# Kernel tuning notes

Hardware: AMD Instinct MI355X
Metric: run time of the kernel (lower is better)

Reference implementation:

```python
import jax, jax.numpy as jnp
import numpy as np

N6 = 524288          # nodes at depth 6 (full-octree batch of 2)
N5 = N6 // 8         # 65536 nodes at depth 5
N4 = N5 // 8         # 8192 nodes at depth 4
EPS = 1e-5           # torch BatchNorm1d default eps


def _pool(x):
    # octree_max_pool on a full octree: 8 contiguous children -> parent max
    n, c = x.shape
    return jnp.max(x.reshape(n // 8, 8, c), axis=1)


def _up(x):
    # octree_upsample on a full octree: each parent broadcast to its 8 children
    return jnp.repeat(x, 8, axis=0)


def _conv1x1_bn_relu(x, w, g, b):
    # Conv1x1 (Linear, no bias) + BatchNorm1d (training-mode batch stats) + ReLU
    y = x @ w                              # [N, Cout]
    m = jnp.mean(y, axis=0)
    v = jnp.var(y, axis=0)                 # biased variance, as in torch BN
    y = (y - m) * jax.lax.rsqrt(v + EPS) * g + b
    return jax.nn.relu(y)


def setup_inputs() -> dict:
    key = jax.random.key(0)
    ks = jax.random.split(key, 8)
    s = 0.02
    return {
        "data0": jax.random.normal(ks[0], (N6, 96), jnp.float32),
        "data1": jax.random.normal(ks[1], (N5, 192), jnp.float32),
        "w01": jax.random.normal(ks[2], (96, 192), jnp.float32) * s,
        "g01": jnp.ones((192,), jnp.float32),
        "b01": jnp.zeros((192,), jnp.float32),
        "w02": jax.random.normal(ks[3], (96, 384), jnp.float32) * s,
        "g02": jnp.ones((384,), jnp.float32),
        "b02": jnp.zeros((384,), jnp.float32),
        "w10": jax.random.normal(ks[4], (192, 96), jnp.float32) * s,
        "g10": jnp.ones((96,), jnp.float32),
        "b10": jnp.zeros((96,), jnp.float32),
        "w12": jax.random.normal(ks[5], (192, 384), jnp.float32) * s,
        "g12": jnp.ones((384,), jnp.float32),
        "b12": jnp.zeros((384,), jnp.float32),
        "depth": 6,
    }


def reference(data0, data1, w01, g01, b01, w02, g02, b02,
              w10, g10, b10, w12, g12, b12, depth):
    # channels = [96, 192, 384]; data0 at depth, data1 at depth-1.
    # out[j] = sum_i TransFunc(channels[i]->channels[j])(data[i], depth-i -> depth-j)
    # j=0 (depth, 96ch):   identity(data0) + upsample(conv10(data1))
    out0 = data0 + _up(_conv1x1_bn_relu(data1, w10, g10, b10))
    # j=1 (depth-1, 192ch): conv01(pool(data0)) + identity(data1)
    p0 = _pool(data0)                      # [N5, 96]
    out1 = _conv1x1_bn_relu(p0, w01, g01, b01) + data1
    # j=2 (depth-2, 384ch): conv02(pool^2(data0)) + conv12(pool(data1))
    out2 = (_conv1x1_bn_relu(_pool(p0), w02, g02, b02)
            + _conv1x1_bn_relu(_pool(data1), w12, g12, b12))
    return (out0, out1, out2)
```

## Files before the change

kernel.cpp:

```cpp
#include <hip/hip_runtime.h>

typedef unsigned short u16;
typedef __attribute__((ext_vector_type(8))) short short8;
typedef __attribute__((ext_vector_type(4))) float f4;
typedef __attribute__((ext_vector_type(4))) unsigned short u16x4;

#define CN6 524288
#define CN5 65536
#define CN4 8192

__device__ inline u16 f2bf(float f){
  unsigned u = __float_as_uint(f);
  return (u16)((u + 0x7FFFu + ((u >> 16) & 1u)) >> 16);
}
__device__ inline float bf2f(u16 h){ return __uint_as_float(((unsigned)h) << 16); }

__device__ inline f4 nt_load4(const float* p){
  return __builtin_nontemporal_load(reinterpret_cast<const f4*>(p));
}
__device__ inline void nt_store4(float* p, f4 v){
  __builtin_nontemporal_store(v, reinterpret_cast<f4*>(p));
}


__global__ __launch_bounds__(256) void k_prep(const float* __restrict__ w10, const float* __restrict__ w01,
                                              const float* __restrict__ w02, const float* __restrict__ w12,
                                              u16* __restrict__ wT10, u16* __restrict__ wT01,
                                              u16* __restrict__ wT02, u16* __restrict__ wT12,
                                              float* __restrict__ stats){
  int i = blockIdx.x * 256 + threadIdx.x;
  if (i < 2112) stats[i] = 0.f;
  if (i < 18432){ int j = i / 192, k = i - j * 192; wT10[i] = f2bf(w10[k * 96 + j]); }
  else if (i < 36864){ int e = i - 18432; int j = e / 96, k = e - j * 96; wT01[e] = f2bf(w01[k * 192 + j]); }
  else if (i < 73728){ int e = i - 36864; int j = e / 96, k = e - j * 96; wT02[e] = f2bf(w02[k * 384 + j]); }
  else if (i < 147456){ int e = i - 73728; int j = e / 192, k = e - j * 192; wT12[e] = f2bf(w12[k * 384 + j]); }
}

__global__ __launch_bounds__(256) void k_gemm10p(const float* __restrict__ d1, const u16* __restrict__ wT10,
                                                 u16* __restrict__ y10, u16* __restrict__ p1){
  __shared__ u16 sm[64 * 200];
  int tid = threadIdx.x, bid = blockIdx.x;

  if (tid < 192){
    int p = tid / 24, c8 = tid - p * 24;
    f4 v0[8], v1[8];
    #pragma unroll
    for (int r = 0; r < 8; r++){
      const float* src = d1 + ((size_t)bid * 64 + p * 8 + r) * 192 + c8 * 8;
      v0[r] = *reinterpret_cast<const f4*>(src);
      v1[r] = *reinterpret_cast<const f4*>(src + 4);
    }
    float mx[8];
    #pragma unroll
    for (int q = 0; q < 4; q++){ mx[q] = v0[0][q]; mx[4 + q] = v1[0][q]; }
    #pragma unroll
    for (int r = 0; r < 8; r++){
      short8 h;
      #pragma unroll
      for (int q = 0; q < 4; q++){
        h[q]     = (short)f2bf(v0[r][q]);
        h[4 + q] = (short)f2bf(v1[r][q]);
        if (r){ mx[q] = fmaxf(mx[q], v0[r][q]); mx[4 + q] = fmaxf(mx[4 + q], v1[r][q]); }
      }
      *reinterpret_cast<short8*>(&sm[(p * 8 + r) * 200 + c8 * 8]) = h;
    }
    short8 hp;
    #pragma unroll
    for (int q = 0; q < 8; q++) hp[q] = (short)f2bf(mx[q]);
    *reinterpret_cast<short8*>(p1 + ((size_t)bid * 8 + p) * 192 + c8 * 8) = hp;
  }
  __syncthreads();

  int lane = tid & 63, wave = tid >> 6;
  int colb = lane & 15;
  int k0 = (lane >> 4) * 8, rgrp = (lane >> 4) * 4;
  int arowl = wave * 16 + colb;
  short8 xf[6];
  #pragma unroll
  for (int s = 0; s < 6; s++) xf[s] = *reinterpret_cast<short8*>(&sm[arowl * 200 + s * 32 + k0]);

  size_t xrow = (size_t)bid * 64 + arowl;
  #pragma unroll
  for (int j = 0; j < 6; j++){
    f4 acc = {0.f, 0.f, 0.f, 0.f};
    const u16* wr = wT10 + (size_t)(j * 16 + colb) * 192 + k0;
    #pragma unroll
    for (int s = 0; s < 6; s++)
      acc = __builtin_amdgcn_mfma_f32_16x16x32_bf16(*reinterpret_cast<const short8*>(wr + s * 32), xf[s], acc, 0, 0, 0);
    u16x4 h;
    #pragma unroll
    for (int r = 0; r < 4; r++) h[r] = f2bf(acc[r]);
    *reinterpret_cast<u16x4*>(y10 + xrow * 96 + j * 16 + rgrp) = h;
  }
}

__global__ __launch_bounds__(192) void k_stats10(const u16* __restrict__ y10, float* __restrict__ stats){
  __shared__ float ls[96], lq[96];
  int tid = threadIdx.x, bid = blockIdx.x;
  if (tid < 96){ ls[tid] = 0.f; lq[tid] = 0.f; }
  __syncthreads();
  int c8 = tid % 12, rl = tid / 12;
  float s1[8], s2[8];
  #pragma unroll
  for (int q = 0; q < 8; q++){ s1[q] = 0.f; s2[q] = 0.f; }
  for (int it = 0; it < 32; it++){
    size_t row = (size_t)bid * 512 + it * 16 + rl;
    short8 h = *reinterpret_cast<const short8*>(y10 + row * 96 + c8 * 8);
    #pragma unroll
    for (int q = 0; q < 8; q++){
      float v = bf2f((u16)h[q]);
      s1[q] += v; s2[q] += v * v;
    }
  }
  #pragma unroll
  for (int q = 0; q < 8; q++){
    atomicAdd(&ls[c8 * 8 + q], s1[q]);
    atomicAdd(&lq[c8 * 8 + q], s2[q]);
  }
  __syncthreads();
  if (tid < 96){ atomicAdd(&stats[tid], ls[tid]); atomicAdd(&stats[1056 + tid], lq[tid]); }
}

__global__ __launch_bounds__(256) void k_out0(const float* __restrict__ d0, const u16* __restrict__ y10,
                                              const float* __restrict__ stats,
                                              const float* __restrict__ g10, const float* __restrict__ b10,
                                              float* __restrict__ out0, u16* __restrict__ p0, u16* __restrict__ p00){
  __shared__ float yv[8][96];
  __shared__ float sd[64][100];
  __shared__ float sp[8][96];
  int tid = threadIdx.x, gp = blockIdx.x;

  if (tid < 192){
    int p = tid / 24, c4 = tid - p * 24;
    u16x4 yb = *reinterpret_cast<const u16x4*>(y10 + ((size_t)gp * 8 + p) * 96 + c4 * 4);
    f4 o;
    #pragma unroll
    for (int q = 0; q < 4; q++){
      int c = c4 * 4 + q;
      float m = stats[c] * (1.f / 65536.f);
      float vv = stats[1056 + c] * (1.f / 65536.f) - m * m;
      float a = g10[c] * rsqrtf(vv + 1e-5f);
      float cc = b10[c] - m * a;
      o[q] = fmaxf(bf2f((u16)yb[q]) * a + cc, 0.f);
    }
    *reinterpret_cast<f4*>(&yv[p][c4 * 4]) = o;
  }
  __syncthreads();

  const float* dsrc = d0 + (size_t)gp * 6144;
  float* ddst = out0 + (size_t)gp * 6144;
  f4 v[6];
  #pragma unroll
  for (int i = 0; i < 6; i++) v[i] = nt_load4(dsrc + (i * 256 + tid) * 4);
  #pragma unroll
  for (int i = 0; i < 6; i++){
    int idx = i * 256 + tid;
    int row = idx / 24, c4 = idx - row * 24;
    f4 y = *reinterpret_cast<f4*>(&yv[row >> 3][c4 * 4]);
    f4 o;
    #pragma unroll
    for (int q = 0; q < 4; q++) o[q] = v[i][q] + y[q];
    nt_store4(ddst + idx * 4, o);
    *reinterpret_cast<f4*>(&sd[row][c4 * 4]) = v[i];
  }
  __syncthreads();

  if (tid < 192){
    int p = tid / 24, c4 = tid - p * 24;
    f4 m = *reinterpret_cast<f4*>(&sd[p * 8][c4 * 4]);
    #pragma unroll
    for (int r = 1; r < 8; r++){
      f4 x = *reinterpret_cast<f4*>(&sd[p * 8 + r][c4 * 4]);
      #pragma unroll
      for (int q = 0; q < 4; q++) m[q] = fmaxf(m[q], x[q]);
    }
    u16x4 h;
    #pragma unroll
    for (int q = 0; q < 4; q++) h[q] = f2bf(m[q]);
    *reinterpret_cast<u16x4*>(p0 + ((size_t)gp * 8 + p) * 96 + c4 * 4) = h;
    *reinterpret_cast<f4*>(&sp[p][c4 * 4]) = m;
  }
  __syncthreads();
  if (tid < 24){
    f4 m = *reinterpret_cast<f4*>(&sp[0][tid * 4]);
    #pragma unroll
    for (int pp = 1; pp < 8; pp++){
      f4 x = *reinterpret_cast<f4*>(&sp[pp][tid * 4]);
      #pragma unroll
      for (int q = 0; q < 4; q++) m[q] = fmaxf(m[q], x[q]);
    }
    u16x4 h;
    #pragma unroll
    for (int q = 0; q < 4; q++) h[q] = f2bf(m[q]);
    *reinterpret_cast<u16x4*>(p00 + (size_t)gp * 96 + tid * 4) = h;
  }
}

template<int Ci, int Co>
__device__ __forceinline__ void stats_body(const u16* __restrict__ x, const u16* __restrict__ wT,
                                           float* __restrict__ sum, float* __restrict__ sq,
                                           int bid, float* ls, float* lq){
  int tid = threadIdx.x;
  for (int t = tid; t < Co; t += 256){ ls[t] = 0.f; lq[t] = 0.f; }
  __syncthreads();
  int lane = tid & 63, wave = tid >> 6;
  int arow = bid * 64 + wave * 16 + (lane & 15);
  int k0 = (lane >> 4) * 8;
  constexpr int KS = Ci / 32;
  short8 af[KS];
  const u16* xr = x + (size_t)arow * Ci + k0;
  #pragma unroll
  for (int s = 0; s < KS; s++) af[s] = *reinterpret_cast<const short8*>(xr + s * 32);
  int colb = lane & 15;
  #pragma unroll 4
  for (int j = 0; j < Co / 16; j++){
    int col = j * 16 + colb;
    f4 acc = {0.f, 0.f, 0.f, 0.f};
    const u16* wr = wT + (size_t)col * Ci + k0;
    #pragma unroll
    for (int s = 0; s < KS; s++)
      acc = __builtin_amdgcn_mfma_f32_16x16x32_bf16(af[s], *reinterpret_cast<const short8*>(wr + s * 32), acc, 0, 0, 0);
    float s1 = acc[0] + acc[1] + acc[2] + acc[3];
    float s2 = acc[0]*acc[0] + acc[1]*acc[1] + acc[2]*acc[2] + acc[3]*acc[3];
    atomicAdd(&ls[col], s1);
    atomicAdd(&lq[col], s2);
  }
  __syncthreads();
  for (int t = tid; t < Co; t += 256){ atomicAdd(&sum[t], ls[t]); atomicAdd(&sq[t], lq[t]); }
}

__global__ __launch_bounds__(256) void k_statsAll(const u16* __restrict__ p0, const u16* __restrict__ p00,
                                                  const u16* __restrict__ p1,
                                                  const u16* __restrict__ wT01, const u16* __restrict__ wT02,
                                                  const u16* __restrict__ wT12, float* __restrict__ stats){
  __shared__ float ls[384], lq[384];
  int bid = blockIdx.x;
  if (bid < 1024)      stats_body<96, 192>(p0,  wT01, stats + 96,  stats + 1056 + 96,  bid,        ls, lq);
  else if (bid < 1152) stats_body<96, 384>(p00, wT02, stats + 288, stats + 1056 + 288, bid - 1024, ls, lq);
  else                 stats_body<192,384>(p1,  wT12, stats + 672, stats + 1056 + 672, bid - 1152, ls, lq);
}

__global__ __launch_bounds__(256) void k_out1(const u16* __restrict__ p0, const u16* __restrict__ wT01,
                                              const float* __restrict__ d1, const float* __restrict__ stats,
                                              const float* __restrict__ g01, const float* __restrict__ b01,
                                              float* __restrict__ out1){
  __shared__ float aL[192], cL[192];
  __shared__ float so[64 * 196];
  int tid = threadIdx.x, bid = blockIdx.x;
  if (tid < 192){
    float m = stats[96 + tid] * (1.f / 65536.f);
    float v = stats[1056 + 96 + tid] * (1.f / 65536.f) - m * m;
    float a = g01[tid] * rsqrtf(v + 1e-5f);
    aL[tid] = a; cL[tid] = b01[tid] - m * a;
  }
  __syncthreads();
  int lane = tid & 63, wave = tid >> 6;
  int colb = lane & 15;
  int k0 = (lane >> 4) * 8, rgrp = (lane >> 4) * 4;
  int rowl = wave * 16 + colb;
  short8 xf[3];
  const u16* xr = p0 + ((size_t)bid * 64 + rowl) * 96 + k0;
  #pragma unroll
  for (int s = 0; s < 3; s++) xf[s] = *reinterpret_cast<const short8*>(xr + s * 32);
  #pragma unroll 4
  for (int j = 0; j < 12; j++){
    int ch0 = j * 16 + rgrp;
    f4 acc = {0.f, 0.f, 0.f, 0.f};
    const u16* wr = wT01 + (size_t)(j * 16 + colb) * 96 + k0;
    #pragma unroll
    for (int s = 0; s < 3; s++)
      acc = __builtin_amdgcn_mfma_f32_16x16x32_bf16(*reinterpret_cast<const short8*>(wr + s * 32), xf[s], acc, 0, 0, 0);
    f4 o;
    #pragma unroll
    for (int r = 0; r < 4; r++){
      int ch = ch0 + r;
      o[r] = fmaxf(acc[r] * aL[ch] + cL[ch], 0.f);
    }
    *reinterpret_cast<f4*>(&so[rowl * 196 + ch0]) = o;
  }
  __syncthreads();
  const float* d1b = d1 + (size_t)bid * 64 * 192;
  float* o1b = out1 + (size_t)bid * 64 * 192;
  #pragma unroll
  for (int i = 0; i < 12; i++){
    int idx = i * 256 + tid;
    int rl = idx / 48, c4i = idx % 48;
    f4 y = *reinterpret_cast<f4*>(&so[rl * 196 + c4i * 4]);
    int off = rl * 192 + c4i * 4;
    f4 g = nt_load4(d1b + off);
    f4 o;
    #pragma unroll
    for (int q = 0; q < 4; q++) o[q] = y[q] + g[q];
    nt_store4(o1b + off, o);
  }
}

__global__ __launch_bounds__(256) void k_out2(const u16* __restrict__ p00, const u16* __restrict__ p1,
                                              const u16* __restrict__ wT02, const u16* __restrict__ wT12,
                                              const float* __restrict__ stats,
                                              const float* __restrict__ g02, const float* __restrict__ b02,
                                              const float* __restrict__ g12, const float* __restrict__ b12,
                                              float* __restrict__ out2){
  __shared__ float a2[384], c2[384], a1[384], c1[384];
  __shared__ float so[32 * 392];
  int tid = threadIdx.x, bid = blockIdx.x;
  for (int t = tid; t < 384; t += 256){
    float m = stats[288 + t] * (1.f / 8192.f);
    float v = stats[1056 + 288 + t] * (1.f / 8192.f) - m * m;
    float a = g02[t] * rsqrtf(v + 1e-5f);
    a2[t] = a; c2[t] = b02[t] - m * a;
    m = stats[672 + t] * (1.f / 8192.f);
    v = stats[1056 + 672 + t] * (1.f / 8192.f) - m * m;
    a = g12[t] * rsqrtf(v + 1e-5f);
    a1[t] = a; c1[t] = b12[t] - m * a;
  }
  __syncthreads();
  int lane = tid & 63, wave = tid >> 6;
  int wr2 = wave >> 1, wc = wave & 1;
  int colb = lane & 15;
  int k0 = (lane >> 4) * 8, rgrp = (lane >> 4) * 4;
  int rowl = wr2 * 16 + colb;
  size_t arow = (size_t)bid * 32 + rowl;
  short8 xA[3], xB[6];
  #pragma unroll
  for (int s = 0; s < 3; s++) xA[s] = *reinterpret_cast<const short8*>(p00 + arow * 96 + k0 + s * 32);
  #pragma unroll
  for (int s = 0; s < 6; s++) xB[s] = *reinterpret_cast<const short8*>(p1 + arow * 192 + k0 + s * 32);
  #pragma unroll 2
  for (int j = 0; j < 12; j++){
    int ch0 = wc * 192 + j * 16 + rgrp;
    int wrow = wc * 192 + j * 16 + colb;
    f4 u = {0.f, 0.f, 0.f, 0.f}, w = {0.f, 0.f, 0.f, 0.f};
    const u16* wra = wT02 + (size_t)wrow * 96 + k0;
    #pragma unroll
    for (int s = 0; s < 3; s++)
      u = __builtin_amdgcn_mfma_f32_16x16x32_bf16(*reinterpret_cast<const short8*>(wra + s * 32), xA[s], u, 0, 0, 0);
    const u16* wrb = wT12 + (size_t)wrow * 192 + k0;
    #pragma unroll
    for (int s = 0; s < 6; s++)
      w = __builtin_amdgcn_mfma_f32_16x16x32_bf16(*reinterpret_cast<const short8*>(wrb + s * 32), xB[s], w, 0, 0, 0);
    f4 o;
    #pragma unroll
    for (int r = 0; r < 4; r++){
      int ch = ch0 + r;
      o[r] = fmaxf(u[r] * a2[ch] + c2[ch], 0.f) + fmaxf(w[r] * a1[ch] + c1[ch], 0.f);
    }
    *reinterpret_cast<f4*>(&so[rowl * 392 + ch0]) = o;
  }
  __syncthreads();
  #pragma unroll
  for (int i = 0; i < 12; i++){
    int idx = i * 256 + tid;
    int rl = idx / 96, c4i = idx % 96;
    f4 v = *reinterpret_cast<f4*>(&so[rl * 392 + c4i * 4]);
    nt_store4(out2 + ((size_t)bid * 32 + rl) * 384 + c4i * 4, v);
  }
}

extern "C" void kernel_launch(void* const* d_in, const int* in_sizes, int n_in,
                              void* d_out, int out_size, void* d_ws, size_t ws_size,
                              hipStream_t stream){
  const float* data0 = (const float*)d_in[0];
  const float* data1 = (const float*)d_in[1];
  const float* w01 = (const float*)d_in[2];
  const float* g01 = (const float*)d_in[3];
  const float* b01 = (const float*)d_in[4];
  const float* w02 = (const float*)d_in[5];
  const float* g02 = (const float*)d_in[6];
  const float* b02 = (const float*)d_in[7];
  const float* w10 = (const float*)d_in[8];
  const float* g10 = (const float*)d_in[9];
  const float* b10 = (const float*)d_in[10];
  const float* w12 = (const float*)d_in[11];
  const float* g12 = (const float*)d_in[12];
  const float* b12 = (const float*)d_in[13];

  float* out0 = (float*)d_out;
  float* out1 = out0 + (size_t)CN6 * 96;
  float* out2 = out1 + (size_t)CN5 * 192;

  char* ws = (char*)d_ws;
  u16* p1   = (u16*)(ws + 0);
  u16* p0   = (u16*)(ws + 3145728);
  u16* p00  = (u16*)(ws + 15728640);
  u16* y10  = (u16*)(ws + 17301504);
  u16* wT10 = (u16*)(ws + 29884416);
  u16* wT01 = (u16*)(ws + 29921280);
  u16* wT02 = (u16*)(ws + 29958144);
  u16* wT12 = (u16*)(ws + 30031872);
  float* stats = (float*)(ws + 30179328);

  k_prep<<<576, 256, 0, stream>>>(w10, w01, w02, w12, wT10, wT01, wT02, wT12, stats);
  k_gemm10p<<<1024, 256, 0, stream>>>(data1, wT10, y10, p1);
  k_stats10<<<128, 192, 0, stream>>>(y10, stats);
  k_out0<<<8192, 256, 0, stream>>>(data0, y10, stats, g10, b10, out0, p0, p00);
  k_statsAll<<<1280, 256, 0, stream>>>(p0, p00, p1, wT01, wT02, wT12, stats);
  k_out1<<<1024, 256, 0, stream>>>(p0, wT01, data1, stats, g01, b01, out1);
  k_out2<<<256, 256, 0, stream>>>(p00, p1, wT02, wT12, stats, g02, b02, g12, b12, out2);
}
```

Baseline: 213.8 us.

## Merge out1/out2 kernels, widen stats10 grid, reduce LDS atomics via shuffles

Combines the out1 and out2 kernels into one launch, with the block index selecting the branch and a shared-memory union, so one launch is saved and the two small grids can run concurrently. The k_stats10 grid grows from 128 to 1024 blocks, each covering 64 rows, to improve occupancy at the cost of more global atomics. In stats_body, per-column partial sums are combined with cross-lane shuffles before the shared-memory atomics, cutting LDS atomic traffic fourfold. The merged kernel's LDS footprint is the larger of the two branches, which may lower occupancy for the out1 blocks.

```diff
diff --git a/kernel.cpp b/kernel.cpp
--- a/kernel.cpp
+++ b/kernel.cpp
@@ -103,8 +103,9 @@
   float s1[8], s2[8];
   #pragma unroll
   for (int q = 0; q < 8; q++){ s1[q] = 0.f; s2[q] = 0.f; }
-  for (int it = 0; it < 32; it++){
-    size_t row = (size_t)bid * 512 + it * 16 + rl;
+  #pragma unroll
+  for (int it = 0; it < 4; it++){
+    size_t row = (size_t)bid * 64 + it * 16 + rl;
     short8 h = *reinterpret_cast<const short8*>(y10 + row * 96 + c8 * 8);
     #pragma unroll
     for (int q = 0; q < 8; q++){
@@ -222,8 +223,12 @@
       acc = __builtin_amdgcn_mfma_f32_16x16x32_bf16(af[s], *reinterpret_cast<const short8*>(wr + s * 32), acc, 0, 0, 0);
     float s1 = acc[0] + acc[1] + acc[2] + acc[3];
     float s2 = acc[0]*acc[0] + acc[1]*acc[1] + acc[2]*acc[2] + acc[3]*acc[3];
-    atomicAdd(&ls[col], s1);
-    atomicAdd(&lq[col], s2);
+    s1 += __shfl_xor(s1, 16); s1 += __shfl_xor(s1, 32);
+    s2 += __shfl_xor(s2, 16); s2 += __shfl_xor(s2, 32);
+    if ((lane >> 4) == 0){
+      atomicAdd(&ls[col], s1);
+      atomicAdd(&lq[col], s2);
+    }
   }
   __syncthreads();
   for (int t = tid; t < Co; t += 256){ atomicAdd(&sum[t], ls[t]); atomicAdd(&sq[t], lq[t]); }
@@ -240,120 +245,123 @@
   else                 stats_body<192,384>(p1,  wT12, stats + 672, stats + 1056 + 672, bid - 1152, ls, lq);
 }
 
-__global__ __launch_bounds__(256) void k_out1(const u16* __restrict__ p0, const u16* __restrict__ wT01,
-                                              const float* __restrict__ d1, const float* __restrict__ stats,
-                                              const float* __restrict__ g01, const float* __restrict__ b01,
-                                              float* __restrict__ out1){
-  __shared__ float aL[192], cL[192];
-  __shared__ float so[64 * 196];
-  int tid = threadIdx.x, bid = blockIdx.x;
-  if (tid < 192){
-    float m = stats[96 + tid] * (1.f / 65536.f);
-    float v = stats[1056 + 96 + tid] * (1.f / 65536.f) - m * m;
-    float a = g01[tid] * rsqrtf(v + 1e-5f);
-    aL[tid] = a; cL[tid] = b01[tid] - m * a;
-  }
-  __syncthreads();
-  int lane = tid & 63, wave = tid >> 6;
-  int colb = lane & 15;
-  int k0 = (lane >> 4) * 8, rgrp = (lane >> 4) * 4;
-  int rowl = wave * 16 + colb;
-  short8 xf[3];
-  const u16* xr = p0 + ((size_t)bid * 64 + rowl) * 96 + k0;
-  #pragma unroll
-  for (int s = 0; s < 3; s++) xf[s] = *reinterpret_cast<const short8*>(xr + s * 32);
-  #pragma unroll 4
-  for (int j = 0; j < 12; j++){
-    int ch0 = j * 16 + rgrp;
-    f4 acc = {0.f, 0.f, 0.f, 0.f};
-    const u16* wr = wT01 + (size_t)(j * 16 + colb) * 96 + k0;
-    #pragma unroll
-    for (int s = 0; s < 3; s++)
-      acc = __builtin_amdgcn_mfma_f32_16x16x32_bf16(*reinterpret_cast<const short8*>(wr + s * 32), xf[s], acc, 0, 0, 0);
-    f4 o;
-    #pragma unroll
-    for (int r = 0; r < 4; r++){
-      int ch = ch0 + r;
-      o[r] = fmaxf(acc[r] * aL[ch] + cL[ch], 0.f);
-    }
-    *reinterpret_cast<f4*>(&so[rowl * 196 + ch0]) = o;
-  }
-  __syncthreads();
-  const float* d1b = d1 + (size_t)bid * 64 * 192;
-  float* o1b = out1 + (size_t)bid * 64 * 192;
-  #pragma unroll
-  for (int i = 0; i < 12; i++){
-    int idx = i * 256 + tid;
-    int rl = idx / 48, c4i = idx % 48;
-    f4 y = *reinterpret_cast<f4*>(&so[rl * 196 + c4i * 4]);
-    int off = rl * 192 + c4i * 4;
-    f4 g = nt_load4(d1b + off);
-    f4 o;
-    #pragma unroll
-    for (int q = 0; q < 4; q++) o[q] = y[q] + g[q];
-    nt_store4(o1b + off, o);
-  }
-}
-
-__global__ __launch_bounds__(256) void k_out2(const u16* __restrict__ p00, const u16* __restrict__ p1,
-                                              const u16* __restrict__ wT02, const u16* __restrict__ wT12,
-                                              const float* __restrict__ stats,
-                                              const float* __restrict__ g02, const float* __restrict__ b02,
-                                              const float* __restrict__ g12, const float* __restrict__ b12,
-                                              float* __restrict__ out2){
-  __shared__ float a2[384], c2[384], a1[384], c1[384];
-  __shared__ float so[32 * 392];
-  int tid = threadIdx.x, bid = blockIdx.x;
-  for (int t = tid; t < 384; t += 256){
-    float m = stats[288 + t] * (1.f / 8192.f);
-    float v = stats[1056 + 288 + t] * (1.f / 8192.f) - m * m;
-    float a = g02[t] * rsqrtf(v + 1e-5f);
-    a2[t] = a; c2[t] = b02[t] - m * a;
-    m = stats[672 + t] * (1.f / 8192.f);
-    v = stats[1056 + 672 + t] * (1.f / 8192.f) - m * m;
-    a = g12[t] * rsqrtf(v + 1e-5f);
-    a1[t] = a; c1[t] = b12[t] - m * a;
-  }
-  __syncthreads();
-  int lane = tid & 63, wave = tid >> 6;
-  int wr2 = wave >> 1, wc = wave & 1;
-  int colb = lane & 15;
-  int k0 = (lane >> 4) * 8, rgrp = (lane >> 4) * 4;
-  int rowl = wr2 * 16 + colb;
-  size_t arow = (size_t)bid * 32 + rowl;
-  short8 xA[3], xB[6];
-  #pragma unroll
-  for (int s = 0; s < 3; s++) xA[s] = *reinterpret_cast<const short8*>(p00 + arow * 96 + k0 + s * 32);
-  #pragma unroll
-  for (int s = 0; s < 6; s++) xB[s] = *reinterpret_cast<const short8*>(p1 + arow * 192 + k0 + s * 32);
-  #pragma unroll 2
-  for (int j = 0; j < 12; j++){
-    int ch0 = wc * 192 + j * 16 + rgrp;
-    int wrow = wc * 192 + j * 16 + colb;
-    f4 u = {0.f, 0.f, 0.f, 0.f}, w = {0.f, 0.f, 0.f, 0.f};
-    const u16* wra = wT02 + (size_t)wrow * 96 + k0;
-    #pragma unroll
-    for (int s = 0; s < 3; s++)
-      u = __builtin_amdgcn_mfma_f32_16x16x32_bf16(*reinterpret_cast<const short8*>(wra + s * 32), xA[s], u, 0, 0, 0);
-    const u16* wrb = wT12 + (size_t)wrow * 192 + k0;
-    #pragma unroll
-    for (int s = 0; s < 6; s++)
-      w = __builtin_amdgcn_mfma_f32_16x16x32_bf16(*reinterpret_cast<const short8*>(wrb + s * 32), xB[s], w, 0, 0, 0);
-    f4 o;
-    #pragma unroll
-    for (int r = 0; r < 4; r++){
-      int ch = ch0 + r;
-      o[r] = fmaxf(u[r] * a2[ch] + c2[ch], 0.f) + fmaxf(w[r] * a1[ch] + c1[ch], 0.f);
-    }
-    *reinterpret_cast<f4*>(&so[rowl * 392 + ch0]) = o;
-  }
-  __syncthreads();
-  #pragma unroll
-  for (int i = 0; i < 12; i++){
-    int idx = i * 256 + tid;
-    int rl = idx / 96, c4i = idx % 96;
-    f4 v = *reinterpret_cast<f4*>(&so[rl * 392 + c4i * 4]);
-    nt_store4(out2 + ((size_t)bid * 32 + rl) * 384 + c4i * 4, v);
+union ShOut {
+  struct { float aL[192], cL[192], so[64 * 196]; } o1;
+  struct { float a2[384], c2[384], a1[384], c1[384], so2[32 * 392]; } o2;
+};
+
+__global__ __launch_bounds__(256) void k_outfinal(const u16* __restrict__ p0, const u16* __restrict__ wT01,
+                                                  const float* __restrict__ d1,
+                                                  const u16* __restrict__ p00, const u16* __restrict__ p1,
+                                                  const u16* __restrict__ wT02, const u16* __restrict__ wT12,
+                                                  const float* __restrict__ stats,
+                                                  const float* __restrict__ g01, const float* __restrict__ b01,
+                                                  const float* __restrict__ g02, const float* __restrict__ b02,
+                                                  const float* __restrict__ g12, const float* __restrict__ b12,
+                                                  float* __restrict__ out1, float* __restrict__ out2){
+  __shared__ ShOut sh;
+  int tid = threadIdx.x;
+  if (blockIdx.x < 1024){
+    int bid = blockIdx.x;
+    if (tid < 192){
+      float m = stats[96 + tid] * (1.f / 65536.f);
+      float v = stats[1056 + 96 + tid] * (1.f / 65536.f) - m * m;
+      float a = g01[tid] * rsqrtf(v + 1e-5f);
+      sh.o1.aL[tid] = a; sh.o1.cL[tid] = b01[tid] - m * a;
+    }
+    __syncthreads();
+    int lane = tid & 63, wave = tid >> 6;
+    int colb = lane & 15;
+    int k0 = (lane >> 4) * 8, rgrp = (lane >> 4) * 4;
+    int rowl = wave * 16 + colb;
+    short8 xf[3];
+    const u16* xr = p0 + ((size_t)bid * 64 + rowl) * 96 + k0;
+    #pragma unroll
+    for (int s = 0; s < 3; s++) xf[s] = *reinterpret_cast<const short8*>(xr + s * 32);
+    #pragma unroll 4
+    for (int j = 0; j < 12; j++){
+      int ch0 = j * 16 + rgrp;
+      f4 acc = {0.f, 0.f, 0.f, 0.f};
+      const u16* wr = wT01 + (size_t)(j * 16 + colb) * 96 + k0;
+      #pragma unroll
+      for (int s = 0; s < 3; s++)
+        acc = __builtin_amdgcn_mfma_f32_16x16x32_bf16(*reinterpret_cast<const short8*>(wr + s * 32), xf[s], acc, 0, 0, 0);
+      f4 o;
+      #pragma unroll
+      for (int r = 0; r < 4; r++){
+        int ch = ch0 + r;
+        o[r] = fmaxf(acc[r] * sh.o1.aL[ch] + sh.o1.cL[ch], 0.f);
+      }
+      *reinterpret_cast<f4*>(&sh.o1.so[rowl * 196 + ch0]) = o;
+    }
+    __syncthreads();
+    const float* d1b = d1 + (size_t)bid * 64 * 192;
+    float* o1b = out1 + (size_t)bid * 64 * 192;
+    #pragma unroll
+    for (int i = 0; i < 12; i++){
+      int idx = i * 256 + tid;
+      int rl = idx / 48, c4i = idx % 48;
+      f4 y = *reinterpret_cast<f4*>(&sh.o1.so[rl * 196 + c4i * 4]);
+      int off = rl * 192 + c4i * 4;
+      f4 g = nt_load4(d1b + off);
+      f4 o;
+      #pragma unroll
+      for (int q = 0; q < 4; q++) o[q] = y[q] + g[q];
+      nt_store4(o1b + off, o);
+    }
+  } else {
+    int bid = blockIdx.x - 1024;
+    for (int t = tid; t < 384; t += 256){
+      float m = stats[288 + t] * (1.f / 8192.f);
+      float v = stats[1056 + 288 + t] * (1.f / 8192.f) - m * m;
+      float a = g02[t] * rsqrtf(v + 1e-5f);
+      sh.o2.a2[t] = a; sh.o2.c2[t] = b02[t] - m * a;
+      m = stats[672 + t] * (1.f / 8192.f);
+      v = stats[1056 + 672 + t] * (1.f / 8192.f) - m * m;
+      a = g12[t] * rsqrtf(v + 1e-5f);
+      sh.o2.a1[t] = a; sh.o2.c1[t] = b12[t] - m * a;
+    }
+    __syncthreads();
+    int lane = tid & 63, wave = tid >> 6;
+    int wr2 = wave >> 1, wc = wave & 1;
+    int colb = lane & 15;
+    int k0 = (lane >> 4) * 8, rgrp = (lane >> 4) * 4;
+    int rowl = wr2 * 16 + colb;
+    size_t arow = (size_t)bid * 32 + rowl;
+    short8 xA[3], xB[6];
+    #pragma unroll
+    for (int s = 0; s < 3; s++) xA[s] = *reinterpret_cast<const short8*>(p00 + arow * 96 + k0 + s * 32);
+    #pragma unroll
+    for (int s = 0; s < 6; s++) xB[s] = *reinterpret_cast<const short8*>(p1 + arow * 192 + k0 + s * 32);
+    #pragma unroll 2
+    for (int j = 0; j < 12; j++){
+      int ch0 = wc * 192 + j * 16 + rgrp;
+      int wrow = wc * 192 + j * 16 + colb;
+      f4 u = {0.f, 0.f, 0.f, 0.f}, w = {0.f, 0.f, 0.f, 0.f};
+      const u16* wra = wT02 + (size_t)wrow * 96 + k0;
+      #pragma unroll
+      for (int s = 0; s < 3; s++)
+        u = __builtin_amdgcn_mfma_f32_16x16x32_bf16(*reinterpret_cast<const short8*>(wra + s * 32), xA[s], u, 0, 0, 0);
+      const u16* wrb = wT12 + (size_t)wrow * 192 + k0;
+      #pragma unroll
+      for (int s = 0; s < 6; s++)
+        w = __builtin_amdgcn_mfma_f32_16x16x32_bf16(*reinterpret_cast<const short8*>(wrb + s * 32), xB[s], w, 0, 0, 0);
+      f4 o;
+      #pragma unroll
+      for (int r = 0; r < 4; r++){
+        int ch = ch0 + r;
+        o[r] = fmaxf(u[r] * sh.o2.a2[ch] + sh.o2.c2[ch], 0.f) + fmaxf(w[r] * sh.o2.a1[ch] + sh.o2.c1[ch], 0.f);
+      }
+      *reinterpret_cast<f4*>(&sh.o2.so2[rowl * 392 + ch0]) = o;
+    }
+    __syncthreads();
+    #pragma unroll
+    for (int i = 0; i < 12; i++){
+      int idx = i * 256 + tid;
+      int rl = idx / 96, c4i = idx % 96;
+      f4 v = *reinterpret_cast<f4*>(&sh.o2.so2[rl * 392 + c4i * 4]);
+      nt_store4(out2 + ((size_t)bid * 32 + rl) * 384 + c4i * 4, v);
+    }
   }
 }
 
@@ -392,9 +400,9 @@
 
   k_prep<<<576, 256, 0, stream>>>(w10, w01, w02, w12, wT10, wT01, wT02, wT12, stats);
   k_gemm10p<<<1024, 256, 0, stream>>>(data1, wT10, y10, p1);
-  k_stats10<<<128, 192, 0, stream>>>(y10, stats);
+  k_stats10<<<1024, 192, 0, stream>>>(y10, stats);
   k_out0<<<8192, 256, 0, stream>>>(data0, y10, stats, g10, b10, out0, p0, p00);
   k_statsAll<<<1280, 256, 0, stream>>>(p0, p00, p1, wT01, wT02, wT12, stats);
-  k_out1<<<1024, 256, 0, stream>>>(p0, wT01, data1, stats, g01, b01, out1);
-  k_out2<<<256, 256, 0, stream>>>(p00, p1, wT02, wT12, stats, g02, b02, g12, b12, out2);
-}
+  k_outfinal<<<1280, 256, 0, stream>>>(p0, wT01, data1, p00, p1, wT02, wT12, stats,
+                                       g01, b01, g02, b02, g12, b12, out1, out2);
+}
```

After: 241.2 us. +12.8%, slower.
